# Kernel optimization log

Measured on AMD Instinct MI355X. Metric: run time of the kernel, lower is better.

Reference implementation:

```python
import jax, jax.numpy as jnp
import numpy as np

NUM_CLASSES = 80
STRIDES = (8, 16, 32)
RADIUS = 2.5
BOX_WEIGHT = 5.0
BIG = 1e9  # emulates restriction of cost/matching to union-candidate anchors
CAND_K = 10


def setup_inputs() -> dict:
    key = jax.random.key(0)
    ks = jax.random.split(key, 6)
    B, G = 16, 16
    p0 = jax.random.normal(ks[0], (B, NUM_CLASSES + 5, 160, 160), jnp.float32)
    p1 = jax.random.normal(ks[1], (B, NUM_CLASSES + 5, 80, 80), jnp.float32)
    p2 = jax.random.normal(ks[2], (B, NUM_CLASSES + 5, 40, 40), jnp.float32)
    cxy = jax.random.uniform(ks[3], (B, G, 2), jnp.float32, 64.0, 1216.0)
    wh = jax.random.uniform(ks[4], (B, G, 2), jnp.float32, 16.0, 256.0)
    cls = jax.random.randint(ks[5], (B, G, 1), 0, NUM_CLASSES).astype(jnp.float32)
    labels = jnp.concatenate([cxy, wh, cls], axis=-1)  # [B,G,5] xywh + class id
    return {"p0": p0, "p1": p1, "p2": p2, "labels": labels}


def _decode(p, stride):
    # [B,C,H,W] -> [B,HW,C] with xy=(xy+grid)*stride, wh=exp(wh)*stride
    B, C, H, W = p.shape
    out = jnp.transpose(p.reshape(B, C, H * W), (0, 2, 1))
    yy, xx = jnp.meshgrid(jnp.arange(H, dtype=p.dtype), jnp.arange(W, dtype=p.dtype), indexing='ij')
    gx, gy = xx.reshape(-1), yy.reshape(-1)
    xy = (out[..., :2] + jnp.stack([gx, gy], axis=-1)) * stride
    wh = jnp.exp(out[..., 2:4]) * stride
    return jnp.concatenate([xy, wh, out[..., 4:]], axis=-1), gx, gy


def _pair_iou(a, b):
    # a:[G,4], b:[A,4] in xywh -> [G,A]
    a1, a2 = a[:, :2] - a[:, 2:] * 0.5, a[:, :2] + a[:, 2:] * 0.5
    b1, b2 = b[:, :2] - b[:, 2:] * 0.5, b[:, :2] + b[:, 2:] * 0.5
    tl = jnp.maximum(a1[:, None], b1[None])
    br = jnp.minimum(a2[:, None], b2[None])
    wh = jnp.maximum(br - tl, 0.0)
    inter = wh[..., 0] * wh[..., 1]
    return inter / (a[:, 2] * a[:, 3])[:, None].__add__((b[:, 2] * b[:, 3])[None]).__sub__(inter).__add__(1e-16)


def _elem_iou(a, b):
    # elementwise xywh iou on [...,4]
    a1, a2 = a[..., :2] - a[..., 2:] * 0.5, a[..., :2] + a[..., 2:] * 0.5
    b1, b2 = b[..., :2] - b[..., 2:] * 0.5, b[..., :2] + b[..., 2:] * 0.5
    wh = jnp.maximum(jnp.minimum(a2, b2) - jnp.maximum(a1, b1), 0.0)
    inter = wh[..., 0] * wh[..., 1]
    return inter / (a[..., 2] * a[..., 3] + b[..., 2] * b[..., 3] - inter + 1e-16)


def _bce_logits(x, t):
    return jnp.maximum(x, 0.0) - x * t + jnp.log1p(jnp.exp(-jnp.abs(x)))


def _assign(tb, tc, pbox, pcls_l, pconf_l, xc, yc, sv):
    # Per-image SimOTA. tb:[G,4] tc:[G] pbox:[A,4] pcls_l:[A,C] pconf_l:[A]
    G = tb.shape[0]
    bx, by, bw, bh = tb[:, 0:1], tb[:, 1:2], tb[:, 2:3], tb[:, 3:4]
    in_box = (xc[None] > bx - bw * 0.5) & (xc[None] < bx + bw * 0.5) & \
             (yc[None] > by - bh * 0.5) & (yc[None] < by + bh * 0.5)  # [G,A]
    r = RADIUS * sv[None]
    in_mir = (xc[None] > bx - r) & (xc[None] < bx + r) & (yc[None] > by - r) & (yc[None] < by + r)
    union = jnp.any(in_box, 0) | jnp.any(in_mir, 0)  # [A]
    inter = in_box & in_mir  # [G,A]
    iou = _pair_iou(tb, pbox)  # [G,A]
    # cls cost: BCE(sqrt(sigmoid(cls)*sigmoid(conf)), one_hot) summed over classes
    p = jnp.sqrt(jax.nn.sigmoid(pcls_l) * jax.nn.sigmoid(pconf_l)[:, None])  # [A,C]
    logp = jnp.clip(jnp.log(p), -100.0, None)
    log1mp = jnp.clip(jnp.log1p(-p), -100.0, None)
    base = -log1mp.sum(-1)  # [A] = sum_c -log(1-p)
    cls_cost = base[None] - logp[:, tc].T + log1mp[:, tc].T  # [G,A]
    cost = cls_cost - 3.0 * jnp.log(iou + 1e-8) + 1e5 * (~inter) + BIG * (~union)[None]
    iou_m = jnp.where(union[None], iou, 0.0)
    dyn_k = jnp.maximum(jax.lax.top_k(iou_m, CAND_K)[0].sum(1).astype(jnp.int32), 1)  # [G]
    _, idx = jax.lax.top_k(-cost, CAND_K)  # per-gt lowest-cost anchors, sorted
    sel = (jnp.arange(CAND_K)[None] < dyn_k[:, None]).astype(cost.dtype)  # [G,K]
    matching = jnp.zeros_like(cost).at[jnp.arange(G)[:, None], idx].max(sel)  # [G,A]
    conflict = matching.sum(0) > 1.0
    gt_min = jnp.argmin(cost, axis=0)  # [A]
    onehot_min = (jnp.arange(G)[:, None] == gt_min[None]).astype(cost.dtype)
    matching = jnp.where(conflict[None], onehot_min, matching)
    fg = matching.sum(0) > 0.0  # [A]
    gidx = jnp.argmax(matching, axis=0)  # [A]
    miou = (matching * iou).sum(0)  # [A]
    t_cls = jax.nn.one_hot(tc[gidx], NUM_CLASSES, dtype=cost.dtype) * miou[:, None]  # [A,C]
    t_box = tb[gidx]  # [A,4]
    return fg, t_cls, t_box


def _forward(p0, p1, p2, labels):
    outs, xcs, ycs, svs = [], [], [], []
    for p, s in zip((p0, p1, p2), STRIDES):
        o, gx, gy = _decode(p, float(s))
        outs.append(o)
        xcs.append((gx + 0.5) * s)
        ycs.append((gy + 0.5) * s)
        svs.append(jnp.full_like(gx, s))
    out = jnp.concatenate(outs, axis=1)  # [B,A,85]
    xc, yc, sv = jnp.concatenate(xcs), jnp.concatenate(ycs), jnp.concatenate(svs)
    pbox, pconf, pcls = out[..., :4], out[..., 4], out[..., 5:]
    tb, tc = labels[..., :4], labels[..., 4].astype(jnp.int32)
    assign = jax.vmap(_assign, in_axes=(0, 0, 0, 0, 0, None, None, None))
    fg, t_cls, t_box = jax.lax.stop_gradient(assign(tb, tc, pbox, pcls, pconf, xc, yc, sv))
    fgf = fg.astype(pbox.dtype)  # target_conf == final fg mask
    loss_box = (fgf * (1.0 - _elem_iou(pbox, t_box) ** 2)).sum()
    loss_conf = _bce_logits(pconf, fgf).sum()
    loss_cls = (fgf[..., None] * _bce_logits(pcls, t_cls)).sum()
    fg_num = jnp.maximum(fgf.sum(), 1.0)
    return (BOX_WEIGHT * loss_box + loss_conf + loss_cls) / fg_num


def reference(p0, p1, p2, labels):
    return _forward(p0, p1, p2, labels)
```

## Files before the change

kernel.cpp:

```cpp
#include <hip/hip_runtime.h>
#include <hip/hip_bf16.h>
#include <cstdint>

#define NCLS 80
#define GNUM 16
#define BNUM 16
#define A0   25600
#define A1   6400
#define A2   1600
#define ATOT 33600
#define QTOT 16800
#define NBLK_A 132
#define NBLK_TOTAL (NBLK_A*BNUM)
#define NSPLIT 8
#define SEG   4200
#define SEG4  1050
#define NWAVE 32
#define FINF  3.4e38f
#define IINF  0x7fffffff

__device__ __forceinline__ float rcpf(float x){ return __builtin_amdgcn_rcpf(x); }
__device__ __forceinline__ float sqf (float x){ return __builtin_amdgcn_sqrtf(x); }
__device__ __forceinline__ float rsqf(float x){ return __builtin_amdgcn_rsqf(x); }

__device__ __forceinline__ float bce(float x, float t){
  float e = __expf(-fabsf(x));
  return fmaxf(x,0.f) - x*t + __logf(1.f + e);
}

__device__ __forceinline__ void get_level(const float* p0, const float* p1, const float* p2,
                                          int a, const float*& p, int& hw, int& off, int& W, float& s)
{
  if (a < A0){ p=p0; hw=A0; off=a; W=160; s=8.f; }
  else if (a < A0+A1){ p=p1; hw=A1; off=a-A0; W=80; s=16.f; }
  else { p=p2; hw=A2; off=a-A0-A1; W=40; s=32.f; }
}

__global__ __launch_bounds__(256, 8) void decode_cost_kernel(
    const float* __restrict__ p0, const float* __restrict__ p1, const float* __restrict__ p2,
    const float* __restrict__ labels,
    float* __restrict__ cost, float4* __restrict__ pbox, float* __restrict__ pconf,
    unsigned char* __restrict__ unionm, unsigned int* __restrict__ match_mask)
{
  const int b = blockIdx.y;
  const int t = threadIdx.x;
  __shared__ float s_tb[GNUM][4];
  __shared__ int   s_tc[GNUM];
  if (t < GNUM){
    const float* L = labels + ((size_t)b*GNUM + t)*5;
    s_tb[t][0]=L[0]; s_tb[t][1]=L[1]; s_tb[t][2]=L[2]; s_tb[t][3]=L[3];
    s_tc[t]=(int)L[4];
  }
  __syncthreads();
  const int q = blockIdx.x*64 + (t>>2);
  const int k = t & 3;
  if (q >= QTOT) return;
  const int a0 = q*2;

  const float* p; int hw, off, W; float s;
  get_level(p0,p1,p2,a0,p,hw,off,W,s);
  const float* bp = p + (size_t)b*(NCLS+5)*hw + off;
  const float* cp = bp + 5*(size_t)hw;

  const float2 RX = *(const float2*)(bp);
  const float2 RY = *(const float2*)(bp + (size_t)hw);
  const float2 RW = *(const float2*)(bp + 2*(size_t)hw);
  const float2 RH = *(const float2*)(bp + 3*(size_t)hw);
  const float2 CL = *(const float2*)(bp + 4*(size_t)hw);

  int gx0 = off % W, gy0 = off / W;
  int gx1 = gx0+1, gy1 = gy0; if (gx1 >= W){ gx1 = 0; gy1++; }

  const float sc0 = rcpf(1.f + __expf(-CL.x));
  const float sc1 = rcpf(1.f + __expf(-CL.y));
  const float ssc0 = sqf(sc0),   ssc1 = sqf(sc1);
  const float rssc0 = rcpf(ssc0), rssc1 = rcpf(ssc1);

  float part0 = 0.f, part1 = 0.f;
  const int cb = 20*k;
  {
    float2 xv[8];
    #pragma unroll
    for (int j=0;j<8;j++) xv[j] = *(const float2*)(cp + (size_t)(cb+j)*hw);
    float pr0=1.f, pr1=1.f;
    #pragma unroll
    for (int j=0;j<8;j++){
      pr0 *= (1.f - ssc0*rsqf(1.f+__expf(-xv[j].x)));
      pr1 *= (1.f - ssc1*rsqf(1.f+__expf(-xv[j].y)));
    }
    part0 -= __logf(pr0); part1 -= __logf(pr1);
  }
  {
    float2 xv[8];
    #pragma unroll
    for (int j=0;j<8;j++) xv[j] = *(const float2*)(cp + (size_t)(cb+8+j)*hw);
    float pr0=1.f, pr1=1.f;
    #pragma unroll
    for (int j=0;j<8;j++){
      pr0 *= (1.f - ssc0*rsqf(1.f+__expf(-xv[j].x)));
      pr1 *= (1.f - ssc1*rsqf(1.f+__expf(-xv[j].y)));
    }
    part0 -= __logf(pr0); part1 -= __logf(pr1);
  }
  {
    float2 xv[4];
    #pragma unroll
    for (int j=0;j<4;j++) xv[j] = *(const float2*)(cp + (size_t)(cb+16+j)*hw);
    float pr0=1.f, pr1=1.f;
    #pragma unroll
    for (int j=0;j<4;j++){
      pr0 *= (1.f - ssc0*rsqf(1.f+__expf(-xv[j].x)));
      pr1 *= (1.f - ssc1*rsqf(1.f+__expf(-xv[j].y)));
    }
    part0 -= __logf(pr0); part1 -= __logf(pr1);
  }
  float base0 = part0 + __shfl_xor(part0, 1); base0 += __shfl_xor(base0, 2);
  float base1 = part1 + __shfl_xor(part1, 1); base1 += __shfl_xor(base1, 2);

  const float px0=(RX.x+gx0)*s, py0=(RY.x+gy0)*s, pw0=__expf(RW.x)*s, ph0=__expf(RH.x)*s;
  const float px1=(RX.y+gx1)*s, py1=(RY.y+gy1)*s, pw1=__expf(RW.y)*s, ph1=__expf(RH.y)*s;
  const float xc0=(gx0+0.5f)*s, yc0=(gy0+0.5f)*s;
  const float xc1=(gx1+0.5f)*s, yc1=(gy1+0.5f)*s;
  const float q1x0=px0-pw0*0.5f, q2x0=px0+pw0*0.5f, q1y0=py0-ph0*0.5f, q2y0=py0+ph0*0.5f;
  const float q1x1=px1-pw1*0.5f, q2x1=px1+pw1*0.5f, q1y1=py1-ph1*0.5f, q2y1=py1+ph1*0.5f;
  const float areaP0 = pw0*ph0, areaP1 = pw1*ph1;
  const float r = 2.5f*s;

  int mybits = 0;
  #pragma unroll
  for (int j=0;j<4;j++){
    const int g = k*4 + j;
    const float bx=s_tb[g][0], by=s_tb[g][1], bw=s_tb[g][2], bh=s_tb[g][3];
    const float b1x=bx-bw*0.5f, b2x=bx+bw*0.5f, b1y=by-bh*0.5f, b2y=by+bh*0.5f;
    const bool u0 = ((xc0>b1x)&&(xc0<b2x)&&(yc0>b1y)&&(yc0<b2y))
                  || ((xc0>bx-r)&&(xc0<bx+r)&&(yc0>by-r)&&(yc0<by+r));
    const bool u1 = ((xc1>b1x)&&(xc1<b2x)&&(yc1>b1y)&&(yc1<b2y))
                  || ((xc1>bx-r)&&(xc1<bx+r)&&(yc1>by-r)&&(yc1<by+r));
    mybits |= (u0?1:0) | (u1?2:0);
  }
  mybits |= __shfl_xor(mybits, 1);
  mybits |= __shfl_xor(mybits, 2);
  const float add0 = (mybits&1)?0.f:1e9f, add1 = (mybits&2)?0.f:1e9f;

  const size_t rowb = (size_t)b*GNUM*ATOT + a0;

  #pragma unroll
  for (int j=0;j<4;j++){
    const int g = k*4 + j;
    const float2 x = *(const float2*)(cp + (size_t)s_tc[g]*hw);
    const float e0 = __expf(-x.x), e1 = __expf(-x.y);
    const float rp0 = rssc0*sqf(1.f+e0), rp1 = rssc1*sqf(1.f+e1);
    const float cd0 = __logf(fmaxf(rp0-1.f, 1e-30f));
    const float cd1 = __logf(fmaxf(rp1-1.f, 1e-30f));

    const float bx=s_tb[g][0], by=s_tb[g][1], bw=s_tb[g][2], bh=s_tb[g][3];
    const float b1x=bx-bw*0.5f, b2x=bx+bw*0.5f, b1y=by-bh*0.5f, b2y=by+bh*0.5f;
    const float areaB = bw*bh;

    const bool inb0 = (xc0>b1x)&&(xc0<b2x)&&(yc0>b1y)&&(yc0<b2y);
    const bool inm0 = (xc0>bx-r)&&(xc0<bx+r)&&(yc0>by-r)&&(yc0<by+r);
    const bool inb1 = (xc1>b1x)&&(xc1<b2x)&&(yc1>b1y)&&(yc1<b2y);
    const bool inm1 = (xc1>bx-r)&&(xc1<bx+r)&&(yc1>by-r)&&(yc1<by+r);

    float iw,ih,inte;
    iw = fmaxf(fminf(b2x,q2x0)-fmaxf(b1x,q1x0),0.f);
    ih = fmaxf(fminf(b2y,q2y0)-fmaxf(b1y,q1y0),0.f);
    inte = iw*ih;
    const float iou0 = inte * rcpf(areaB+areaP0-inte+1e-16f);
    iw = fmaxf(fminf(b2x,q2x1)-fmaxf(b1x,q1x1),0.f);
    ih = fmaxf(fminf(b2y,q2y1)-fmaxf(b1y,q1y1),0.f);
    inte = iw*ih;
    const float iou1 = inte * rcpf(areaB+areaP1-inte+1e-16f);

    float2 cst;
    cst.x = base0 + cd0 - 3.f*__logf(iou0+1e-8f) + ((inb0&&inm0)?0.f:100000.f) + add0;
    cst.y = base1 + cd1 - 3.f*__logf(iou1+1e-8f) + ((inb1&&inm1)?0.f:100000.f) + add1;
    *(float2*)(cost + rowb + (size_t)g*ATOT) = cst;
  }

  if (k == 0){
    pbox[(size_t)b*ATOT+a0  ] = make_float4(px0,py0,pw0,ph0);
    pbox[(size_t)b*ATOT+a0+1] = make_float4(px1,py1,pw1,ph1);
    *(float2*)(pconf + (size_t)b*ATOT + a0) = make_float2(CL.x, CL.y);
    uchar2 um; um.x = (mybits&1)?1:0; um.y = (mybits&2)?1:0;
    *(uchar2*)(unionm + (size_t)b*ATOT + a0) = um;
    uint2 z; z.x = 0u; z.y = 0u;
    *(uint2*)(match_mask + (size_t)b*ATOT + a0) = z;
  }
}

__global__ __launch_bounds__(256) void topk_stage1(
    const float* __restrict__ cost, const float4* __restrict__ pbox,
    const unsigned char* __restrict__ unionm, const float* __restrict__ labels,
    float* __restrict__ cand_c, int* __restrict__ cand_i, float* __restrict__ cand_v)
{
  const int bg   = blockIdx.y;
  const int b    = bg >> 4;
  const int seg  = blockIdx.x;
  const int wave = threadIdx.x >> 6;
  const int lane = threadIdx.x & 63;
  const int wg   = seg*4 + wave;

  const float4* crow4 = (const float4*)(cost + (size_t)bg*ATOT);
  const uchar4* urow4 = (const uchar4*)(unionm + (size_t)b*ATOT);
  const float4* prow  = pbox + (size_t)b*ATOT;
  const float bx = labels[bg*5+0], by = labels[bg*5+1];
  const float bw = labels[bg*5+2], bh = labels[bg*5+3];
  const float areaB = bw*bh;
  const float b1x=bx-bw*0.5f, b2x=bx+bw*0.5f, b1y=by-bh*0.5f, b2y=by+bh*0.5f;

  const int slot0 = seg*SEG4;

  float cv[10]; int ci[10]; float iv[10];
  #pragma unroll
  for (int k=0;k<10;k++){ cv[k]=FINF; ci[k]=IINF; iv[k]=0.f; }

  for (int sl = threadIdx.x; sl < SEG4; sl += 256){
    const int slot = slot0 + sl;
    const float4 c4 = crow4[slot];
    const int abase = slot*4;
    #pragma unroll
    for (int j=0;j<4;j++){
      const float c = (j==0)?c4.x:(j==1)?c4.y:(j==2)?c4.z:c4.w;
      const int a = abase + j;
      if (c < cv[9] || (c == cv[9] && a < ci[9])){
        float nc=c; int ni=a;
        #pragma unroll
        for (int k=0;k<10;k++){
          bool better = (nc < cv[k]) || (nc==cv[k] && ni<ci[k]);
          float tv=cv[k]; int ti=ci[k];
          cv[k]=better?nc:cv[k]; ci[k]=better?ni:ci[k];
          nc  =better?tv:nc;     ni  =better?ti:ni;
        }
      }
    }
    const uchar4 u4 = urow4[slot];
    if (u4.x | u4.y | u4.z | u4.w){
      #pragma unroll
      for (int j=0;j<4;j++){
        const unsigned char uf = (j==0)?u4.x:(j==1)?u4.y:(j==2)?u4.z:u4.w;
        if (uf){
          const float4 pb = prow[abase + j];
          float tlx=fmaxf(b1x, pb.x-pb.z*0.5f), brx=fminf(b2x, pb.x+pb.z*0.5f);
          float tly=fmaxf(b1y, pb.y-pb.w*0.5f), bry=fminf(b2y, pb.y+pb.w*0.5f);
          float iw=fmaxf(brx-tlx,0.f), ih=fmaxf(bry-tly,0.f);
          float inte=iw*ih;
          float io = inte * rcpf(areaB + pb.z*pb.w - inte + 1e-16f);
          if (io > iv[9]){
            float nv=io;
            #pragma unroll
            for (int k=0;k<10;k++){
              bool better = nv > iv[k];
              float tv=iv[k];
              iv[k]=better?nv:iv[k];
              nv  =better?tv:nv;
            }
          }
        }
      }
    }
  }

  float selc = 0.f; int seli = 0;
  #pragma unroll
  for (int r=0;r<10;r++){
    float bv = cv[0]; int bi = ci[0];
    #pragma unroll
    for (int off=32; off>0; off>>=1){
      float ov = __shfl_xor(bv, off);
      int   oi = __shfl_xor(bi, off);
      bool take = (ov < bv) || (ov==bv && oi<bi);
      bv = take?ov:bv; bi = take?oi:bi;
    }
    if (lane == r){ selc = bv; seli = bi; }
    if (cv[0]==bv && ci[0]==bi){
      #pragma unroll
      for (int k=0;k<9;k++){ cv[k]=cv[k+1]; ci[k]=ci[k+1]; }
      cv[9]=FINF; ci[9]=IINF;
    }
  }
  float selv = 0.f;
  #pragma unroll
  for (int r=0;r<10;r++){
    float bv = iv[0]; int bl = lane;
    #pragma unroll
    for (int off=32; off>0; off>>=1){
      float ov = __shfl_xor(bv, off);
      int   ol = __shfl_xor(bl, off);
      bool take = (ov > bv) || (ov==bv && ol<bl);
      bv = take?ov:bv; bl = take?ol:bl;
    }
    if (lane == r) selv = bv;
    if (lane == bl){
      #pragma unroll
      for (int k=0;k<9;k++){ iv[k]=iv[k+1]; }
      iv[9]=0.f;
    }
  }

  if (lane < 10){
    const size_t base = ((size_t)bg*NWAVE + wg)*10 + lane;
    cand_c[base] = selc;
    cand_i[base] = seli;
    cand_v[base] = selv;
  }
}

__global__ __launch_bounds__(64) void topk_stage2(
    const float* __restrict__ cand_c, const int* __restrict__ cand_i,
    const float* __restrict__ cand_v, unsigned int* __restrict__ match_mask)
{
  const int bg = blockIdx.x;
  const int b = bg >> 4, g = bg & 15;
  const int lane = threadIdx.x;
  const size_t base = (size_t)bg*NWAVE*10 + lane*5;

  float cv[5]; int ci[5]; float iv[5];
  #pragma unroll
  for (int k=0;k<5;k++){ cv[k]=cand_c[base+k]; ci[k]=cand_i[base+k]; iv[k]=cand_v[base+k]; }

  int seli = 0;
  #pragma unroll
  for (int r=0;r<10;r++){
    float bv = cv[0]; int bi = ci[0];
    #pragma unroll
    for (int off=32; off>0; off>>=1){
      float ov = __shfl_xor(bv, off);
      int   oi = __shfl_xor(bi, off);
      bool take = (ov < bv) || (ov==bv && oi<bi);
      bv = take?ov:bv; bi = take?oi:bi;
    }
    if (lane == r) seli = bi;
    if (cv[0]==bv && ci[0]==bi){
      #pragma unroll
      for (int k=0;k<4;k++){ cv[k]=cv[k+1]; ci[k]=ci[k+1]; }
      cv[4]=FINF; ci[4]=IINF;
    }
  }

  float isum = 0.f;
  #pragma unroll
  for (int r=0;r<10;r++){
    float bv = iv[0]; int bl = lane;
    #pragma unroll
    for (int off=32; off>0; off>>=1){
      float ov = __shfl_xor(bv, off);
      int   ol = __shfl_xor(bl, off);
      bool take = (ov > bv) || (ov==bv && ol<bl);
      bv = take?ov:bv; bl = take?ol:bl;
    }
    isum += bv;
    if (lane == bl){
      #pragma unroll
      for (int k=0;k<4;k++){ iv[k]=iv[k+1]; }
      iv[4]=0.f;
    }
  }

  int dynk = (int)isum;
  if (dynk < 1)  dynk = 1;
  if (dynk > 10) dynk = 10;
  if (lane < dynk)
    atomicOr(&match_mask[(size_t)b*ATOT + seli], 1u<<g);
}

__global__ __launch_bounds__(256) void loss_kernel(
    const float* __restrict__ p0, const float* __restrict__ p1, const float* __restrict__ p2,
    const float* __restrict__ labels,
    const float* __restrict__ cost, const float4* __restrict__ pbox,
    const float* __restrict__ pconf, const unsigned int* __restrict__ match_mask,
    float* __restrict__ blocksums)
{
  const int b = blockIdx.y;
  const int a = blockIdx.x*256 + threadIdx.x;
  float lbox=0.f, lconf=0.f, lcls=0.f, fgn=0.f;
  if (a < ATOT){
    unsigned int m = match_mask[(size_t)b*ATOT+a];
    float cl = pconf[(size_t)b*ATOT+a];
    if (m != 0u){
      int gidx;
      if (__popc(m) > 1){
        float best = FINF; int bgi = 0;
        for (int g=0; g<GNUM; g++){
          float c = cost[((size_t)b*GNUM+g)*ATOT + a];
          if (c < best){ best=c; bgi=g; }
        }
        gidx = bgi;
      } else {
        gidx = __ffs(m)-1;
      }
      const float* L = labels + ((size_t)b*GNUM+gidx)*5;
      float bx=L[0], by=L[1], bw=L[2], bh=L[3];
      int tcg=(int)L[4];
      float4 pb = pbox[(size_t)b*ATOT+a];
      float tlx=fmaxf(bx-bw*0.5f, pb.x-pb.z*0.5f);
      float brx=fminf(bx+bw*0.5f, pb.x+pb.z*0.5f);
      float tly=fmaxf(by-bh*0.5f, pb.y-pb.w*0.5f);
      float bry=fminf(by+bh*0.5f, pb.y+pb.w*0.5f);
      float iw=fmaxf(brx-tlx,0.f), ih=fmaxf(bry-tly,0.f);
      float inte=iw*ih;
      float iou = inte * rcpf(bw*bh + pb.z*pb.w - inte + 1e-16f);
      lbox = 1.f - iou*iou;
      lconf = bce(cl, 1.f);
      float miou = iou;
      const float* p; int hw, off, W; float s;
      get_level(p0,p1,p2,a,p,hw,off,W,s);
      const float* bp = p + (size_t)b*(NCLS+5)*hw + off;
      for (int c=0;c<NCLS;c++){
        float x = bp[(size_t)(5+c)*hw];
        float t = (c==tcg)? miou : 0.f;
        lcls += bce(x, t);
      }
      fgn = 1.f;
    } else {
      lconf = bce(cl, 0.f);
    }
  }
  #pragma unroll
  for (int off2=32; off2>0; off2>>=1){
    lbox  += __shfl_down(lbox,  off2);
    lconf += __shfl_down(lconf, off2);
    lcls  += __shfl_down(lcls,  off2);
    fgn   += __shfl_down(fgn,   off2);
  }
  __shared__ float s_red[4][4];
  const int wave = threadIdx.x >> 6;
  if ((threadIdx.x & 63)==0){
    s_red[wave][0]=lbox; s_red[wave][1]=lconf; s_red[wave][2]=lcls; s_red[wave][3]=fgn;
  }
  __syncthreads();
  if (threadIdx.x==0){
    float r0=0,r1=0,r2=0,r3=0;
    #pragma unroll
    for (int w=0;w<4;w++){ r0+=s_red[w][0]; r1+=s_red[w][1]; r2+=s_red[w][2]; r3+=s_red[w][3]; }
    const int bid = blockIdx.y*gridDim.x + blockIdx.x;
    ((float4*)blocksums)[bid] = make_float4(r0,r1,r2,r3);
  }
}

__global__ __launch_bounds__(256) void finalize_kernel(
    const float* __restrict__ blocksums, float* __restrict__ out)
{
  const int tid = threadIdx.x;
  float r0=0,r1=0,r2=0,r3=0;
  for (int i = tid; i < NBLK_TOTAL; i += 256){
    const float4 v = ((const float4*)blocksums)[i];
    r0+=v.x; r1+=v.y; r2+=v.z; r3+=v.w;
  }
  #pragma unroll
  for (int off=32; off>0; off>>=1){
    r0 += __shfl_down(r0, off);
    r1 += __shfl_down(r1, off);
    r2 += __shfl_down(r2, off);
    r3 += __shfl_down(r3, off);
  }
  __shared__ float s_red[4][4];
  const int wave = tid >> 6;
  if ((tid & 63)==0){ s_red[wave][0]=r0; s_red[wave][1]=r1; s_red[wave][2]=r2; s_red[wave][3]=r3; }
  __syncthreads();
  if (tid==0){
    float t0=0,t1=0,t2=0,t3=0;
    #pragma unroll
    for (int w=0;w<4;w++){ t0+=s_red[w][0]; t1+=s_red[w][1]; t2+=s_red[w][2]; t3+=s_red[w][3]; }
    out[0] = (5.f*t0 + t1 + t2) / fmaxf(t3, 1.f);
  }
}

extern "C" void kernel_launch(void* const* d_in, const int* in_sizes, int n_in,
                              void* d_out, int out_size, void* d_ws, size_t ws_size,
                              hipStream_t stream)
{
  const float* p0     = (const float*)d_in[0];
  const float* p1     = (const float*)d_in[1];
  const float* p2     = (const float*)d_in[2];
  const float* labels = (const float*)d_in[3];

  char* ws = (char*)d_ws;
  size_t o = 0;
  float*        cost       = (float*)(ws + o);        o += (size_t)BNUM*GNUM*ATOT*4;
  float4*       pbox       = (float4*)(ws + o);       o += (size_t)BNUM*ATOT*16;
  float*        pconf      = (float*)(ws + o);        o += (size_t)BNUM*ATOT*4;
  unsigned int* match_mask = (unsigned int*)(ws + o); o += (size_t)BNUM*ATOT*4;
  unsigned char* unionm    = (unsigned char*)(ws + o);o += (size_t)BNUM*ATOT;
  o = (o + 255) & ~(size_t)255;
  float*        blocksums  = (float*)(ws + o);        o += (size_t)NBLK_TOTAL*4*4;
  o = (o + 255) & ~(size_t)255;
  float*        cand_c     = (float*)(ws + o);        o += (size_t)256*NWAVE*10*4;
  int*          cand_i     = (int*)(ws + o);          o += (size_t)256*NWAVE*10*4;
  float*        cand_v     = (float*)(ws + o);        o += (size_t)256*NWAVE*10*4;

  dim3 gridA((QTOT + 63)/64, BNUM);
  decode_cost_kernel<<<gridA, 256, 0, stream>>>(p0,p1,p2,labels,cost,pbox,pconf,unionm,match_mask);
  dim3 gridT(NSPLIT, BNUM*GNUM);
  topk_stage1<<<gridT, 256, 0, stream>>>(cost, pbox, unionm, labels, cand_c, cand_i, cand_v);
  topk_stage2<<<BNUM*GNUM, 64, 0, stream>>>(cand_c, cand_i, cand_v, match_mask);
  dim3 gridC(NBLK_A, BNUM);
  loss_kernel<<<gridC, 256, 0, stream>>>(p0,p1,p2,labels,cost,pbox,pconf,match_mask,blocksums);
  finalize_kernel<<<1, 256, 0, stream>>>(blocksums, (float*)d_out);
}
```

Measured before the change: 139.2 us.

## Fuse two-stage top-k into one kernel with shared-memory merge

Merges the two top-k kernels into one launch of 256 blocks of 1024 threads. Each of 16 waves scans a slice of the cost row and writes its top-10 candidates to shared memory, then wave 0 merges them and sets the match mask. This removes a kernel launch and the global round trip for candidate arrays. In exchange, parallelism drops from 2048 blocks of 256 threads to 256 blocks of 1024, and the final merge runs on a single wave per block.

```diff
diff --git a/kernel.cpp b/kernel.cpp
--- a/kernel.cpp
+++ b/kernel.cpp
@@ -12,10 +12,8 @@
 #define QTOT 16800
 #define NBLK_A 132
 #define NBLK_TOTAL (NBLK_A*BNUM)
-#define NSPLIT 8
-#define SEG   4200
-#define SEG4  1050
-#define NWAVE 32
+#define SLOT_TOT 8400
+#define WSEG4 525
 #define FINF  3.4e38f
 #define IINF  0x7fffffff
 
@@ -184,22 +182,20 @@
     *(float2*)(pconf + (size_t)b*ATOT + a0) = make_float2(CL.x, CL.y);
     uchar2 um; um.x = (mybits&1)?1:0; um.y = (mybits&2)?1:0;
     *(uchar2*)(unionm + (size_t)b*ATOT + a0) = um;
-    uint2 z; z.x = 0u; z.y = 0u;
+    uint2 z; z.x=0u; z.y=0u;
     *(uint2*)(match_mask + (size_t)b*ATOT + a0) = z;
   }
 }
 
-__global__ __launch_bounds__(256) void topk_stage1(
+__global__ __launch_bounds__(1024) void topk_fused(
     const float* __restrict__ cost, const float4* __restrict__ pbox,
     const unsigned char* __restrict__ unionm, const float* __restrict__ labels,
-    float* __restrict__ cand_c, int* __restrict__ cand_i, float* __restrict__ cand_v)
-{
-  const int bg   = blockIdx.y;
-  const int b    = bg >> 4;
-  const int seg  = blockIdx.x;
+    unsigned int* __restrict__ match_mask)
+{
+  const int bg = blockIdx.x;
+  const int b = bg >> 4, g = bg & 15;
   const int wave = threadIdx.x >> 6;
   const int lane = threadIdx.x & 63;
-  const int wg   = seg*4 + wave;
 
   const float4* crow4 = (const float4*)(cost + (size_t)bg*ATOT);
   const uchar4* urow4 = (const uchar4*)(unionm + (size_t)b*ATOT);
@@ -209,14 +205,13 @@
   const float areaB = bw*bh;
   const float b1x=bx-bw*0.5f, b2x=bx+bw*0.5f, b1y=by-bh*0.5f, b2y=by+bh*0.5f;
 
-  const int slot0 = seg*SEG4;
-
   float cv[10]; int ci[10]; float iv[10];
   #pragma unroll
   for (int k=0;k<10;k++){ cv[k]=FINF; ci[k]=IINF; iv[k]=0.f; }
 
-  for (int sl = threadIdx.x; sl < SEG4; sl += 256){
-    const int slot = slot0 + sl;
+  const int slot0 = wave*WSEG4;
+  for (int s2 = lane; s2 < WSEG4; s2 += 64){
+    const int slot = slot0 + s2;
     const float4 c4 = crow4[slot];
     const int abase = slot*4;
     #pragma unroll
@@ -261,6 +256,7 @@
     }
   }
 
+  __shared__ float s_c[16][10]; __shared__ int s_i[16][10]; __shared__ float s_v[16][10];
   float selc = 0.f; int seli = 0;
   #pragma unroll
   for (int r=0;r<10;r++){
@@ -297,71 +293,56 @@
       iv[9]=0.f;
     }
   }
-
-  if (lane < 10){
-    const size_t base = ((size_t)bg*NWAVE + wg)*10 + lane;
-    cand_c[base] = selc;
-    cand_i[base] = seli;
-    cand_v[base] = selv;
-  }
-}
-
-__global__ __launch_bounds__(64) void topk_stage2(
-    const float* __restrict__ cand_c, const int* __restrict__ cand_i,
-    const float* __restrict__ cand_v, unsigned int* __restrict__ match_mask)
-{
-  const int bg = blockIdx.x;
-  const int b = bg >> 4, g = bg & 15;
-  const int lane = threadIdx.x;
-  const size_t base = (size_t)bg*NWAVE*10 + lane*5;
-
-  float cv[5]; int ci[5]; float iv[5];
-  #pragma unroll
-  for (int k=0;k<5;k++){ cv[k]=cand_c[base+k]; ci[k]=cand_i[base+k]; iv[k]=cand_v[base+k]; }
-
-  int seli = 0;
-  #pragma unroll
-  for (int r=0;r<10;r++){
-    float bv = cv[0]; int bi = ci[0];
-    #pragma unroll
-    for (int off=32; off>0; off>>=1){
-      float ov = __shfl_xor(bv, off);
-      int   oi = __shfl_xor(bi, off);
-      bool take = (ov < bv) || (ov==bv && oi<bi);
-      bv = take?ov:bv; bi = take?oi:bi;
-    }
-    if (lane == r) seli = bi;
-    if (cv[0]==bv && ci[0]==bi){
+  if (lane < 10){ s_c[wave][lane]=selc; s_i[wave][lane]=seli; s_v[wave][lane]=selv; }
+  __syncthreads();
+
+  if (wave == 0){
+    const int list = lane>>2, ch = lane&3;
+    const int st  = (ch<2)? ch*3 : 6 + (ch-2)*2;
+    const int len = (ch<2)? 3 : 2;
+    float c3[3]; int i3[3]; float v3[3];
+    #pragma unroll
+    for (int j=0;j<3;j++){
+      c3[j] = (j<len)? s_c[list][st+j] : FINF;
+      i3[j] = (j<len)? s_i[list][st+j] : IINF;
+      v3[j] = (j<len)? s_v[list][st+j] : 0.f;
+    }
+    int sel2 = 0;
+    #pragma unroll
+    for (int r=0;r<10;r++){
+      float bv = c3[0]; int bi = i3[0];
       #pragma unroll
-      for (int k=0;k<4;k++){ cv[k]=cv[k+1]; ci[k]=ci[k+1]; }
-      cv[4]=FINF; ci[4]=IINF;
-    }
-  }
-
-  float isum = 0.f;
-  #pragma unroll
-  for (int r=0;r<10;r++){
-    float bv = iv[0]; int bl = lane;
-    #pragma unroll
-    for (int off=32; off>0; off>>=1){
-      float ov = __shfl_xor(bv, off);
-      int   ol = __shfl_xor(bl, off);
-      bool take = (ov > bv) || (ov==bv && ol<bl);
-      bv = take?ov:bv; bl = take?ol:bl;
-    }
-    isum += bv;
-    if (lane == bl){
+      for (int off=32; off>0; off>>=1){
+        float ov = __shfl_xor(bv, off);
+        int   oi = __shfl_xor(bi, off);
+        bool take = (ov < bv) || (ov==bv && oi<bi);
+        bv = take?ov:bv; bi = take?oi:bi;
+      }
+      if (lane == r) sel2 = bi;
+      if (c3[0]==bv && i3[0]==bi){
+        c3[0]=c3[1]; i3[0]=i3[1]; c3[1]=c3[2]; i3[1]=i3[2]; c3[2]=FINF; i3[2]=IINF;
+      }
+    }
+    float isum = 0.f;
+    #pragma unroll
+    for (int r=0;r<10;r++){
+      float bv = v3[0]; int bl = lane;
       #pragma unroll
-      for (int k=0;k<4;k++){ iv[k]=iv[k+1]; }
-      iv[4]=0.f;
-    }
-  }
-
-  int dynk = (int)isum;
-  if (dynk < 1)  dynk = 1;
-  if (dynk > 10) dynk = 10;
-  if (lane < dynk)
-    atomicOr(&match_mask[(size_t)b*ATOT + seli], 1u<<g);
+      for (int off=32; off>0; off>>=1){
+        float ov = __shfl_xor(bv, off);
+        int   ol = __shfl_xor(bl, off);
+        bool take = (ov > bv) || (ov==bv && ol<bl);
+        bv = take?ov:bv; bl = take?ol:bl;
+      }
+      isum += bv;
+      if (lane == bl){ v3[0]=v3[1]; v3[1]=v3[2]; v3[2]=0.f; }
+    }
+    int dynk = (int)isum;
+    if (dynk < 1)  dynk = 1;
+    if (dynk > 10) dynk = 10;
+    if (lane < dynk)
+      atomicOr(&match_mask[(size_t)b*ATOT + sel2], 1u<<g);
+  }
 }
 
 __global__ __launch_bounds__(256) void loss_kernel(
@@ -484,16 +465,10 @@
   unsigned char* unionm    = (unsigned char*)(ws + o);o += (size_t)BNUM*ATOT;
   o = (o + 255) & ~(size_t)255;
   float*        blocksums  = (float*)(ws + o);        o += (size_t)NBLK_TOTAL*4*4;
-  o = (o + 255) & ~(size_t)255;
-  float*        cand_c     = (float*)(ws + o);        o += (size_t)256*NWAVE*10*4;
-  int*          cand_i     = (int*)(ws + o);          o += (size_t)256*NWAVE*10*4;
-  float*        cand_v     = (float*)(ws + o);        o += (size_t)256*NWAVE*10*4;
 
   dim3 gridA((QTOT + 63)/64, BNUM);
   decode_cost_kernel<<<gridA, 256, 0, stream>>>(p0,p1,p2,labels,cost,pbox,pconf,unionm,match_mask);
-  dim3 gridT(NSPLIT, BNUM*GNUM);
-  topk_stage1<<<gridT, 256, 0, stream>>>(cost, pbox, unionm, labels, cand_c, cand_i, cand_v);
-  topk_stage2<<<BNUM*GNUM, 64, 0, stream>>>(cand_c, cand_i, cand_v, match_mask);
+  topk_fused<<<BNUM*GNUM, 1024, 0, stream>>>(cost, pbox, unionm, labels, match_mask);
   dim3 gridC(NBLK_A, BNUM);
   loss_kernel<<<gridC, 256, 0, stream>>>(p0,p1,p2,labels,cost,pbox,pconf,match_mask,blocksums);
   finalize_kernel<<<1, 256, 0, stream>>>(blocksums, (float*)d_out);
```

New measurement: 142.0 us. About the same (+2.0%).
